# Kernel tuning notes

Measured on AMD Instinct MI355X. Metric: run time of the kernel, lower is better.

The kernel has to match this reference:

```python
import jax, jax.numpy as jnp
import numpy as np

EMBED_DIM = 1024
NUM_HEADS = 16
D_K = EMBED_DIM // NUM_HEADS


def setup_inputs() -> dict:
    key = jax.random.key(0)
    ks = jax.random.split(key, 5)
    x = jax.random.normal(ks[0], (2, 2048, EMBED_DIM), dtype=jnp.float32)
    # kaiming_normal on 2D params: std = sqrt(2/fan_in) with fan_in = in_features
    w_qkv = jax.random.normal(ks[1], (3 * EMBED_DIM, EMBED_DIM), dtype=jnp.float32) * np.sqrt(2.0 / EMBED_DIM)
    b_qkv = jnp.zeros((3 * EMBED_DIM,), dtype=jnp.float32)
    w_o = jax.random.normal(ks[2], (EMBED_DIM, EMBED_DIM), dtype=jnp.float32) * np.sqrt(2.0 / EMBED_DIM)
    b_o = jnp.zeros((EMBED_DIM,), dtype=jnp.float32)
    return {"x": x, "w_qkv": w_qkv, "b_qkv": b_qkv, "w_o": w_o, "b_o": b_o}


def reference(x, w_qkv, b_qkv, w_o, b_o):
    B, N, C = x.shape
    qkv = x @ w_qkv.T + b_qkv  # [B,N,3C]
    q, k, v = jnp.split(qkv, 3, axis=-1)
    # [B,H,N,d_k]
    q = q.reshape(B, N, NUM_HEADS, D_K).transpose(0, 2, 1, 3)
    k = k.reshape(B, N, NUM_HEADS, D_K).transpose(0, 2, 1, 3)
    v = v.reshape(B, N, NUM_HEADS, D_K).transpose(0, 2, 1, 3)
    # NOTE: original forward scales by 1/sqrt(embed_dim), not 1/sqrt(d_k)
    scores = jnp.einsum('bhqd,bhkd->bhqk', q, k) / np.sqrt(C).astype(np.float32)
    causal = jnp.tril(jnp.ones((N, N), dtype=bool))
    scores = jnp.where(causal, scores, -jnp.inf)
    attn = jax.nn.softmax(scores, axis=-1)
    out = jnp.einsum('bhqk,bhkd->bhqd', attn, v)  # [B,H,N,d_k]
    out = out.transpose(0, 2, 1, 3).reshape(B, N, C)
    return out @ w_o.T + b_o
```

## Files before the change

kernel.cpp:

```cpp
#include <hip/hip_runtime.h>
#include <hip/hip_bf16.h>
#include <math.h>

typedef __bf16 bf16_t;
typedef __bf16 bf16x8 __attribute__((ext_vector_type(8)));
typedef __bf16 bf16x4 __attribute__((ext_vector_type(4)));
typedef __bf16 bf16x2 __attribute__((ext_vector_type(2)));
typedef float f32x4 __attribute__((ext_vector_type(4)));
typedef unsigned u32x4 __attribute__((ext_vector_type(4)));

#define SCALE_L2E 0.045084234f
#define ROUND_B 0.0028169f

#define MFMA16(a, b, c) __builtin_amdgcn_mfma_f32_16x16x32_bf16(a, b, c, 0, 0, 0)

__device__ __forceinline__ unsigned pack2(float a, float b) {
  return __builtin_amdgcn_perm(__builtin_bit_cast(unsigned, b),
                               __builtin_bit_cast(unsigned, a), 0x07060302u);
}

__global__ void convert3_f32_bf16(const float* __restrict__ a, int na,
                                  const float* __restrict__ b, int nb,
                                  const float* __restrict__ c, int nc,
                                  bf16_t* __restrict__ oa, bf16_t* __restrict__ ob,
                                  bf16_t* __restrict__ oc) {
  int i = (blockIdx.x * blockDim.x + threadIdx.x) * 8;
  const float* src;
  bf16_t* dst;
  int off;
  if (i < na) { src = a; dst = oa; off = i; }
  else if (i < na + nb) { src = b; dst = ob; off = i - na; }
  else if (i < na + nb + nc) { src = c; dst = oc; off = i - na - nb; }
  else return;
  float4 u = *(const float4*)&src[off];
  float4 v = *(const float4*)&src[off + 4];
  bf16x8 w = {(bf16_t)u.x, (bf16_t)u.y, (bf16_t)u.z, (bf16_t)u.w,
              (bf16_t)v.x, (bf16_t)v.y, (bf16_t)v.z, (bf16_t)v.w};
  *(bf16x8*)&dst[off] = w;
}

#define GLOBAL_AS __attribute__((address_space(1)))
#define LDS_AS __attribute__((address_space(3)))
__device__ __forceinline__ void g2l16(const void* g, void* l) {
  __builtin_amdgcn_global_load_lds((const GLOBAL_AS void*)g, (LDS_AS void*)l,
                                   16, 0, 0);
}

template <typename TC, int BN>
__launch_bounds__(256)
__global__ void gemm_bt_bias(const bf16_t* __restrict__ A,
                             const bf16_t* __restrict__ B,
                             const float* __restrict__ bias,
                             TC* __restrict__ C,
                             int M, int N, int K) {
  constexpr int NT = BN / 32;
  __shared__ bf16_t As[128 * 32];
  __shared__ bf16_t Bs[BN * 32];

  const int t = threadIdx.x;
  const int wave = t >> 6, lane = t & 63, quad = lane >> 4, ln = lane & 15;
  const int wm = (wave >> 1) * 64, wn = (wave & 1) * (BN / 2);
  const int m0 = blockIdx.y * 128, n0 = blockIdx.x * BN;

  const int srow = lane >> 2;
  const int schunk = ((lane & 3) ^ ((lane >> 3) & 3)) * 8;
  const bf16_t* gA0 = &A[(size_t)(m0 + wave * 32 + srow) * K + schunk];
  const bf16_t* gA1 = gA0 + (size_t)16 * K;
  bf16_t* lA0 = &As[(wave * 32) * 32];
  bf16_t* lA1 = &As[(wave * 32 + 16) * 32];
  const bf16_t* gB0 = &B[(size_t)(n0 + (BN == 128 ? wave * 32 : wave * 16) + srow) * K + schunk];
  const bf16_t* gB1 = gB0 + (size_t)16 * K;
  bf16_t* lB0 = &Bs[((BN == 128 ? wave * 32 : wave * 16)) * 32];
  bf16_t* lB1 = &Bs[(wave * 32 + 16) * 32];

  const int cslot = (quad ^ ((ln >> 1) & 3)) * 8;

  f32x4 acc[4][NT];
  for (int i = 0; i < 4; i++)
    for (int j = 0; j < NT; j++) acc[i][j] = (f32x4){0.f, 0.f, 0.f, 0.f};

  for (int k0 = 0; k0 < K; k0 += 32) {
    __syncthreads();
    g2l16(gA0 + k0, lA0);
    g2l16(gA1 + k0, lA1);
    g2l16(gB0 + k0, lB0);
    if (BN == 128) g2l16(gB1 + k0, lB1);
    __syncthreads();

    bf16x8 af[4], bfr[NT];
    for (int mt = 0; mt < 4; mt++)
      af[mt] = *(const bf16x8*)&As[(wm + mt * 16 + ln) * 32 + cslot];
    for (int nt = 0; nt < NT; nt++)
      bfr[nt] = *(const bf16x8*)&Bs[(wn + nt * 16 + ln) * 32 + cslot];
    for (int mt = 0; mt < 4; mt++)
      for (int nt = 0; nt < NT; nt++)
        acc[mt][nt] = MFMA16(af[mt], bfr[nt], acc[mt][nt]);
  }

  for (int nt = 0; nt < NT; nt++) {
    int col = n0 + wn + nt * 16 + ln;
    float bv = bias[col];
    for (int mt = 0; mt < 4; mt++) {
      int row = m0 + wm + mt * 16 + quad * 4;
      for (int r = 0; r < 4; r++)
        C[(size_t)(row + r) * N + col] = (TC)(acc[mt][nt][r] + bv);
    }
  }
}

__launch_bounds__(256, 2)
__global__ void gemm128db(const bf16_t* __restrict__ A,
                          const bf16_t* __restrict__ B,
                          const float* __restrict__ bias,
                          bf16_t* __restrict__ C,
                          int M, int N, int K) {
  __shared__ __align__(16) bf16_t Ab[2][128 * 64];
  __shared__ __align__(16) bf16_t Bb[2][128 * 64];

  const int tid = threadIdx.x;
  const int wave = tid >> 6, lane = tid & 63, quad = lane >> 4, ln = lane & 15;
  const int wm = wave >> 1, wn = wave & 1;
  const int m0 = blockIdx.y * 128, n0 = blockIdx.x * 128;
  const int nt = K >> 6;

  const int rowoff = wave * 8 + (lane >> 3);
  const int c8 = ((lane & 7) ^ (lane >> 3)) * 8;
  const int w8row = wave * 8;
  const bf16_t* Arow0 = A + (size_t)(m0 + rowoff) * K + c8;
  const bf16_t* Brow0 = B + (size_t)(n0 + rowoff) * K + c8;

  auto stA = [&](int tl) {
    const bf16_t* g = Arow0 + (size_t)tl * 64;
    bf16_t* l = &Ab[tl & 1][w8row * 64];
#pragma unroll
    for (int rr = 0; rr < 128; rr += 32)
      g2l16(g + (size_t)rr * K, l + rr * 64);
  };
  auto stB = [&](int tl) {
    const bf16_t* g = Brow0 + (size_t)tl * 64;
    bf16_t* l = &Bb[tl & 1][w8row * 64];
#pragma unroll
    for (int rr = 0; rr < 128; rr += 32)
      g2l16(g + (size_t)rr * K, l + rr * 64);
  };

  const int cswl = (quad ^ (ln & 7)) * 8;
  const int aBase = (wm * 64 + ln) * 64;
  const int bBase = (wn * 64 + ln) * 64;

  f32x4 acc[4][4];
#pragma unroll
  for (int i = 0; i < 4; i++)
#pragma unroll
    for (int j = 0; j < 4; j++) acc[i][j] = (f32x4){0.f, 0.f, 0.f, 0.f};

  bf16x8 af[4][2], bfr[4][2];

  auto ldA = [&](int buf) {
#pragma unroll
    for (int mf = 0; mf < 4; ++mf)
#pragma unroll
      for (int sk = 0; sk < 2; ++sk)
        af[mf][sk] = *(const bf16x8*)&Ab[buf][aBase + mf * 1024 +
                                             (cswl ^ (sk << 5))];
  };
  auto ldB = [&](int buf) {
#pragma unroll
    for (int nf = 0; nf < 4; ++nf)
#pragma unroll
      for (int sk = 0; sk < 2; ++sk)
        bfr[nf][sk] = *(const bf16x8*)&Bb[buf][bBase + nf * 1024 +
                                               (cswl ^ (sk << 5))];
  };
  auto mm = [&]() {
#pragma unroll
    for (int mf = 0; mf < 4; ++mf)
#pragma unroll
      for (int nf = 0; nf < 4; ++nf) {
        f32x4 c = acc[mf][nf];
        c = MFMA16(af[mf][0], bfr[nf][0], c);
        c = MFMA16(af[mf][1], bfr[nf][1], c);
        acc[mf][nf] = c;
      }
  };

  stA(0); stB(0);
  __syncthreads();

  for (int tl = 0; tl < nt; ++tl) {
    const int buf = tl & 1;
    if (tl + 1 < nt) { stA(tl + 1); stB(tl + 1); }
    ldA(buf);
    ldB(buf);
    mm();
    __syncthreads();
  }

#pragma unroll
  for (int nf = 0; nf < 4; ++nf) {
    const int col = n0 + wn * 64 + nf * 16 + ln;
    const float bv = bias[col];
#pragma unroll
    for (int mf = 0; mf < 4; ++mf) {
      const int row = m0 + wm * 64 + mf * 16 + quad * 4;
#pragma unroll
      for (int r = 0; r < 4; ++r)
        C[(size_t)(row + r) * N + col] = (bf16_t)(acc[mf][nf][r] + bv);
    }
  }
}

__launch_bounds__(256, 2)
__global__ void attn_kernel(const bf16_t* __restrict__ qkv,
                            bf16_t* __restrict__ out) {
  constexpr int KP = 72, VP = 72;
  constexpr int BUF = 64 * KP;
  __shared__ __align__(16) bf16_t KsB[2 * BUF];
  __shared__ __align__(16) bf16_t VtB[2 * BUF];

  const int t = threadIdx.x;
  const int wave = t >> 6, lane = t & 63, quad = lane >> 4, ln = lane & 15;
  const int p = blockIdx.x >> 5;
  const int bh = blockIdx.x & 31;
  const int b = bh >> 4, h = bh & 15;
  const int qA = p * 64, qB = (31 - p) * 64;
  const int ntiles = 32 - p;
  const size_t rs = 3072;
  const size_t base = (size_t)b * 2048 * rs;

  const size_t qoffA = base + (size_t)(qA + wave * 16 + ln) * rs + h * 64;
  const size_t qoffB = base + (size_t)(qB + wave * 16 + ln) * rs + h * 64;
  bf16x8 qfA0 = *(const bf16x8*)&qkv[qoffA + quad * 8];
  bf16x8 qfA1 = *(const bf16x8*)&qkv[qoffA + 32 + quad * 8];
  bf16x8 qfB0 = *(const bf16x8*)&qkv[qoffB + quad * 8];
  bf16x8 qfB1 = *(const bf16x8*)&qkv[qoffB + 32 + quad * 8];

  f32x4 oA[4], oB[4];
  f32x4 lAv = (f32x4){0.f, 0.f, 0.f, 0.f};
  f32x4 lBv = (f32x4){0.f, 0.f, 0.f, 0.f};
  for (int ct = 0; ct < 4; ct++) {
    oA[ct] = (f32x4){0.f, 0.f, 0.f, 0.f};
    oB[ct] = (f32x4){0.f, 0.f, 0.f, 0.f};
  }

  const int r0 = t >> 3, c0 = (t & 7) * 8;
  const int ksA = r0 * KP + (((t & 7) + wave) & 7) * 8;
  const int ksB2 = (r0 + 32) * KP + (((t & 7) + wave + 4) & 7) * 8;
  const int vkoff = ((((r0 >> 2) + (t & 7)) & 7)) * 8 + 2 * (r0 & 3);

  const bf16_t* kpa = &qkv[base + 1024 + h * 64 + (size_t)r0 * rs + c0];
  const bf16_t* kpb = kpa + (size_t)32 * rs;
  const bf16_t* vpa = &qkv[base + 2048 + h * 64 + (size_t)(2 * r0) * rs + c0];
  const bf16_t* vpb = vpa + rs;
  const size_t tstep = (size_t)64 * rs;

  bf16x8 ka = *(const bf16x8*)kpa; kpa += tstep;
  bf16x8 kb = *(const bf16x8*)kpb; kpb += tstep;
  bf16x8 va2 = *(const bf16x8*)vpa; vpa += tstep;
  bf16x8 vb2 = *(const bf16x8*)vpb; vpb += tstep;

  const int qgA = qA + wave * 16 + ln;
  const int qgB = qB + wave * 16 + ln;

  auto stage_to = [&](int buf) {
    bf16_t* KsW = &KsB[buf * BUF];
    bf16_t* VtW = &VtB[buf * BUF];
    *(bf16x8*)&KsW[ksA] = ka;
    *(bf16x8*)&KsW[ksB2] = kb;
#pragma unroll
    for (int j = 0; j < 8; j++) {
      bf16x2 w2 = {va2[j], vb2[j]};
      *(bf16x2*)&VtW[(c0 + j) * VP + vkoff] = w2;
    }
  };
  auto prefetch = [&]() {
    ka = *(const bf16x8*)kpa; kpa += tstep;
    kb = *(const bf16x8*)kpb; kpb += tstep;
    va2 = *(const bf16x8*)vpa; vpa += tstep;
    vb2 = *(const bf16x8*)vpb; vpb += tstep;
  };
  auto load_kfs = [&](const bf16_t* Ks, bf16x8* kf0s, bf16x8* kf1s) {
#pragma unroll
    for (int st = 0; st < 4; st++) {
      const int krow = st * 16 + ln;
      const int rot = 2 * st + (ln >> 3);
      kf0s[st] = *(const bf16x8*)&Ks[krow * KP + ((quad + rot) & 7) * 8];
      kf1s[st] = *(const bf16x8*)&Ks[krow * KP + ((quad + 4 + rot) & 7) * 8];
    }
  };
  auto qk_block = [&](const bf16x8* kf0s, const bf16x8* kf1s, bf16x8 q0,
                      bf16x8 q1, f32x4& lxv, bf16x8* Bp, bool masked,
                      int kbase, int qg) {
#pragma unroll
    for (int pr = 0; pr < 2; pr++) {
      u32x4 u;
#pragma unroll
      for (int sh = 0; sh < 2; sh++) {
        const int st = pr * 2 + sh;
        f32x4 s = (f32x4){0.f, 0.f, 0.f, 0.f};
        __builtin_amdgcn_s_setprio(1);
        s = MFMA16(kf0s[st], q0, s);
        s = MFMA16(kf1s[st], q1, s);
        __builtin_amdgcn_s_setprio(0);
        const int k0g = kbase + st * 16 + quad * 4;
        float pv[4];
#pragma unroll
        for (int r = 0; r < 4; r++) {
          float e = __builtin_amdgcn_exp2f(fmaf(s[r], SCALE_L2E, ROUND_B));
          if (masked && (k0g + r > qg)) e = 0.f;
          lxv[r] += e;
          pv[r] = e;
        }
        u[sh * 2] = pack2(pv[0], pv[1]);
        u[sh * 2 + 1] = pack2(pv[2], pv[3]);
      }
      Bp[pr] = __builtin_bit_cast(bf16x8, u);
    }
  };
  auto load_vfs = [&](const bf16_t* Vt, bf16x8* A8s) {
#pragma unroll
    for (int pr = 0; pr < 2; pr++) {
#pragma unroll
      for (int ct = 0; ct < 4; ct++) {
        const int dd = ct * 16 + ln;
        const int bc = (quad >> 1) + 2 * ct + (ln >> 3);
        const int cA = (4 * pr + bc) & 7;
        const int cB = (4 * pr + 2 + bc) & 7;
        bf16x4 v0 = *(const bf16x4*)&Vt[dd * VP + cA * 8 + (quad & 1) * 4];
        bf16x4 v1 = *(const bf16x4*)&Vt[dd * VP + cB * 8 + (quad & 1) * 4];
        A8s[pr * 4 + ct] = __builtin_shufflevector(v0, v1, 0, 1, 2, 3, 4, 5, 6, 7);
      }
    }
  };

  auto body = [&](int kt, bool hasA, bool maskA, bool maskB) {
    if (kt + 1 < ntiles) {
      stage_to((kt + 1) & 1);
      if (kt + 2 < ntiles) prefetch();
    }
    const bf16_t* Ks = &KsB[(kt & 1) * BUF];
    const bf16_t* Vt = &VtB[(kt & 1) * BUF];
    bf16x8 kf0s[4], kf1s[4];
    load_kfs(Ks, kf0s, kf1s);
    bf16x8 BpA[2], BpB[2];
    if (hasA) qk_block(kf0s, kf1s, qfA0, qfA1, lAv, BpA, maskA, kt * 64, qgA);
    qk_block(kf0s, kf1s, qfB0, qfB1, lBv, BpB, maskB, kt * 64, qgB);
    bf16x8 A8s[8];
    load_vfs(Vt, A8s);
    __builtin_amdgcn_s_setprio(1);
#pragma unroll
    for (int pr = 0; pr < 2; pr++) {
#pragma unroll
      for (int ct = 0; ct < 4; ct++) {
        if (hasA) oA[ct] = MFMA16(A8s[pr * 4 + ct], BpA[pr], oA[ct]);
        oB[ct] = MFMA16(A8s[pr * 4 + ct], BpB[pr], oB[ct]);
      }
    }
    __builtin_amdgcn_s_setprio(0);
    if (kt + 1 < ntiles) __syncthreads();
  };

  stage_to(0);
  if (ntiles > 1) prefetch();
  __syncthreads();

  for (int kt = 0; kt < p; kt++) body(kt, true, false, false);
  body(p, true, true, false);
  for (int kt = p + 1; kt < 31 - p; kt++) body(kt, false, false, false);
  body(31 - p, false, false, true);

  float lAx = (lAv[0] + lAv[1]) + (lAv[2] + lAv[3]);
  float lBx = (lBv[0] + lBv[1]) + (lBv[2] + lBv[3]);
  lAx += __shfl_xor(lAx, 16);
  lAx += __shfl_xor(lAx, 32);
  lBx += __shfl_xor(lBx, 16);
  lBx += __shfl_xor(lBx, 32);
  const float invA = __builtin_amdgcn_rcpf(lAx);
  const float invB = __builtin_amdgcn_rcpf(lBx);
  const int ocol = h * 64 + quad * 4;
#pragma unroll
  for (int ct = 0; ct < 4; ct++) {
    bf16x4 wa, wb;
#pragma unroll
    for (int r = 0; r < 4; r++) {
      wa[r] = (bf16_t)(oA[ct][r] * invA);
      wb[r] = (bf16_t)(oB[ct][r] * invB);
    }
    *(bf16x4*)&out[(size_t)(b * 2048 + qgA) * 1024 + ocol + ct * 16] = wa;
    *(bf16x4*)&out[(size_t)(b * 2048 + qgB) * 1024 + ocol + ct * 16] = wb;
  }
}

extern "C" void kernel_launch(void* const* d_in, const int* in_sizes, int n_in,
                              void* d_out, int out_size, void* d_ws, size_t ws_size,
                              hipStream_t stream) {
  const float* x     = (const float*)d_in[0];
  const float* w_qkv = (const float*)d_in[1];
  const float* b_qkv = (const float*)d_in[2];
  const float* w_o   = (const float*)d_in[3];
  const float* b_o   = (const float*)d_in[4];
  float* out = (float*)d_out;

  bf16_t* qkv   = (bf16_t*)d_ws;
  bf16_t* xbf   = qkv + (size_t)4096 * 3072;
  bf16_t* wqkvb = xbf + (size_t)4096 * 1024;
  bf16_t* wob   = wqkvb + (size_t)3072 * 1024;
  bf16_t* attn  = xbf;

  const int na = 4096 * 1024, nb = 3072 * 1024, nc = 1024 * 1024;
  convert3_f32_bf16<<<dim3((na + nb + nc) / (256 * 8)), 256, 0, stream>>>(
      x, na, w_qkv, nb, w_o, nc, xbf, wqkvb, wob);

  gemm128db<<<dim3(3072 / 128, 4096 / 128), 256, 0, stream>>>(
      xbf, wqkvb, b_qkv, qkv, 4096, 3072, 1024);
  attn_kernel<<<dim3(512), 256, 0, stream>>>(qkv, attn);
  gemm_bt_bias<float, 64><<<dim3(1024 / 64, 4096 / 128), 256, 0, stream>>>(
      attn, wob, b_o, out, 4096, 1024, 1024);
}
```

Before: 177.7 us.

## Split each attention key tile across two wave groups with LDS reduction

The attention block grows from 256 to 512 threads, and each half of the waves handles half of every 64-key tile. In the global-to-LDS staging, one half loads K and the other loads V. Each half now computes half the QK and PV MFMAs per tile, holding fewer K/V fragments per wave. The halves' partial outputs and row sums are combined through LDS at the end. The goal is more waves per CU to hide latency and shorter per-wave dependency chains, at the cost of an extra barrier, an LDS reduction, and a tighter register budget under the new launch bounds.

```diff
diff --git a/kernel.cpp b/kernel.cpp
--- a/kernel.cpp
+++ b/kernel.cpp
@@ -210,7 +210,7 @@
   }
 }
 
-__launch_bounds__(256, 2)
+__launch_bounds__(512, 4)
 __global__ void attn_kernel(const bf16_t* __restrict__ qkv,
                             bf16_t* __restrict__ out) {
   constexpr int KP = 72, VP = 72;
@@ -220,6 +220,8 @@
 
   const int t = threadIdx.x;
   const int wave = t >> 6, lane = t & 63, quad = lane >> 4, ln = lane & 15;
+  const int qw = wave & 3;
+  const int kh = wave >> 2;
   const int p = blockIdx.x >> 5;
   const int bh = blockIdx.x & 31;
   const int b = bh >> 4, h = bh & 15;
@@ -228,8 +230,8 @@
   const size_t rs = 3072;
   const size_t base = (size_t)b * 2048 * rs;
 
-  const size_t qoffA = base + (size_t)(qA + wave * 16 + ln) * rs + h * 64;
-  const size_t qoffB = base + (size_t)(qB + wave * 16 + ln) * rs + h * 64;
+  const size_t qoffA = base + (size_t)(qA + qw * 16 + ln) * rs + h * 64;
+  const size_t qoffB = base + (size_t)(qB + qw * 16 + ln) * rs + h * 64;
   bf16x8 qfA0 = *(const bf16x8*)&qkv[qoffA + quad * 8];
   bf16x8 qfA1 = *(const bf16x8*)&qkv[qoffA + 32 + quad * 8];
   bf16x8 qfB0 = *(const bf16x8*)&qkv[qoffB + quad * 8];
@@ -243,93 +245,93 @@
     oB[ct] = (f32x4){0.f, 0.f, 0.f, 0.f};
   }
 
-  const int r0 = t >> 3, c0 = (t & 7) * 8;
-  const int ksA = r0 * KP + (((t & 7) + wave) & 7) * 8;
-  const int ksB2 = (r0 + 32) * KP + (((t & 7) + wave + 4) & 7) * 8;
-  const int vkoff = ((((r0 >> 2) + (t & 7)) & 7)) * 8 + 2 * (r0 & 3);
-
-  const bf16_t* kpa = &qkv[base + 1024 + h * 64 + (size_t)r0 * rs + c0];
-  const bf16_t* kpb = kpa + (size_t)32 * rs;
-  const bf16_t* vpa = &qkv[base + 2048 + h * 64 + (size_t)(2 * r0) * rs + c0];
-  const bf16_t* vpb = vpa + rs;
+  const int t256 = t & 255;
+  const int r0 = t256 >> 3, c0 = (t256 & 7) * 8;
+  const int wav4 = t256 >> 6;
+  const int ksA = r0 * KP + (((t256 & 7) + wav4) & 7) * 8;
+  const int ksB2 = (r0 + 32) * KP + (((t256 & 7) + wav4 + 4) & 7) * 8;
+  const int vkoff = ((((r0 >> 2) + (t256 & 7)) & 7)) * 8 + 2 * (r0 & 3);
+
+  const bf16_t* gp0;
+  const bf16_t* gp1;
+  if (kh) {
+    gp0 = &qkv[base + 1024 + h * 64 + (size_t)r0 * rs + c0];
+    gp1 = gp0 + (size_t)32 * rs;
+  } else {
+    gp0 = &qkv[base + 2048 + h * 64 + (size_t)(2 * r0) * rs + c0];
+    gp1 = gp0 + rs;
+  }
   const size_t tstep = (size_t)64 * rs;
 
-  bf16x8 ka = *(const bf16x8*)kpa; kpa += tstep;
-  bf16x8 kb = *(const bf16x8*)kpb; kpb += tstep;
-  bf16x8 va2 = *(const bf16x8*)vpa; vpa += tstep;
-  bf16x8 vb2 = *(const bf16x8*)vpb; vpb += tstep;
-
-  const int qgA = qA + wave * 16 + ln;
-  const int qgB = qB + wave * 16 + ln;
+  bf16x8 s0 = *(const bf16x8*)gp0; gp0 += tstep;
+  bf16x8 s1 = *(const bf16x8*)gp1; gp1 += tstep;
+
+  const int qgA = qA + qw * 16 + ln;
+  const int qgB = qB + qw * 16 + ln;
 
   auto stage_to = [&](int buf) {
-    bf16_t* KsW = &KsB[buf * BUF];
-    bf16_t* VtW = &VtB[buf * BUF];
-    *(bf16x8*)&KsW[ksA] = ka;
-    *(bf16x8*)&KsW[ksB2] = kb;
-#pragma unroll
-    for (int j = 0; j < 8; j++) {
-      bf16x2 w2 = {va2[j], vb2[j]};
-      *(bf16x2*)&VtW[(c0 + j) * VP + vkoff] = w2;
+    if (kh) {
+      bf16_t* KsW = &KsB[buf * BUF];
+      *(bf16x8*)&KsW[ksA] = s0;
+      *(bf16x8*)&KsW[ksB2] = s1;
+    } else {
+      bf16_t* VtW = &VtB[buf * BUF];
+#pragma unroll
+      for (int j = 0; j < 8; j++) {
+        bf16x2 w2 = {s0[j], s1[j]};
+        *(bf16x2*)&VtW[(c0 + j) * VP + vkoff] = w2;
+      }
     }
   };
   auto prefetch = [&]() {
-    ka = *(const bf16x8*)kpa; kpa += tstep;
-    kb = *(const bf16x8*)kpb; kpb += tstep;
-    va2 = *(const bf16x8*)vpa; vpa += tstep;
-    vb2 = *(const bf16x8*)vpb; vpb += tstep;
+    s0 = *(const bf16x8*)gp0; gp0 += tstep;
+    s1 = *(const bf16x8*)gp1; gp1 += tstep;
   };
   auto load_kfs = [&](const bf16_t* Ks, bf16x8* kf0s, bf16x8* kf1s) {
 #pragma unroll
-    for (int st = 0; st < 4; st++) {
+    for (int sh = 0; sh < 2; sh++) {
+      const int st = kh * 2 + sh;
       const int krow = st * 16 + ln;
       const int rot = 2 * st + (ln >> 3);
-      kf0s[st] = *(const bf16x8*)&Ks[krow * KP + ((quad + rot) & 7) * 8];
-      kf1s[st] = *(const bf16x8*)&Ks[krow * KP + ((quad + 4 + rot) & 7) * 8];
+      kf0s[sh] = *(const bf16x8*)&Ks[krow * KP + ((quad + rot) & 7) * 8];
+      kf1s[sh] = *(const bf16x8*)&Ks[krow * KP + ((quad + 4 + rot) & 7) * 8];
     }
   };
   auto qk_block = [&](const bf16x8* kf0s, const bf16x8* kf1s, bf16x8 q0,
-                      bf16x8 q1, f32x4& lxv, bf16x8* Bp, bool masked,
+                      bf16x8 q1, f32x4& lxv, bf16x8& Bp, bool masked,
                       int kbase, int qg) {
-#pragma unroll
-    for (int pr = 0; pr < 2; pr++) {
-      u32x4 u;
-#pragma unroll
-      for (int sh = 0; sh < 2; sh++) {
-        const int st = pr * 2 + sh;
-        f32x4 s = (f32x4){0.f, 0.f, 0.f, 0.f};
-        __builtin_amdgcn_s_setprio(1);
-        s = MFMA16(kf0s[st], q0, s);
-        s = MFMA16(kf1s[st], q1, s);
-        __builtin_amdgcn_s_setprio(0);
-        const int k0g = kbase + st * 16 + quad * 4;
-        float pv[4];
-#pragma unroll
-        for (int r = 0; r < 4; r++) {
-          float e = __builtin_amdgcn_exp2f(fmaf(s[r], SCALE_L2E, ROUND_B));
-          if (masked && (k0g + r > qg)) e = 0.f;
-          lxv[r] += e;
-          pv[r] = e;
-        }
-        u[sh * 2] = pack2(pv[0], pv[1]);
-        u[sh * 2 + 1] = pack2(pv[2], pv[3]);
+    u32x4 u;
+#pragma unroll
+    for (int sh = 0; sh < 2; sh++) {
+      f32x4 s = (f32x4){0.f, 0.f, 0.f, 0.f};
+      __builtin_amdgcn_s_setprio(1);
+      s = MFMA16(kf0s[sh], q0, s);
+      s = MFMA16(kf1s[sh], q1, s);
+      __builtin_amdgcn_s_setprio(0);
+      const int k0g = kbase + (kh * 2 + sh) * 16 + quad * 4;
+      float pv[4];
+#pragma unroll
+      for (int r = 0; r < 4; r++) {
+        float e = __builtin_amdgcn_exp2f(fmaf(s[r], SCALE_L2E, ROUND_B));
+        if (masked && (k0g + r > qg)) e = 0.f;
+        lxv[r] += e;
+        pv[r] = e;
       }
-      Bp[pr] = __builtin_bit_cast(bf16x8, u);
-    }
+      u[sh * 2] = pack2(pv[0], pv[1]);
+      u[sh * 2 + 1] = pack2(pv[2], pv[3]);
+    }
+    Bp = __builtin_bit_cast(bf16x8, u);
   };
   auto load_vfs = [&](const bf16_t* Vt, bf16x8* A8s) {
 #pragma unroll
-    for (int pr = 0; pr < 2; pr++) {
-#pragma unroll
-      for (int ct = 0; ct < 4; ct++) {
-        const int dd = ct * 16 + ln;
-        const int bc = (quad >> 1) + 2 * ct + (ln >> 3);
-        const int cA = (4 * pr + bc) & 7;
-        const int cB = (4 * pr + 2 + bc) & 7;
-        bf16x4 v0 = *(const bf16x4*)&Vt[dd * VP + cA * 8 + (quad & 1) * 4];
-        bf16x4 v1 = *(const bf16x4*)&Vt[dd * VP + cB * 8 + (quad & 1) * 4];
-        A8s[pr * 4 + ct] = __builtin_shufflevector(v0, v1, 0, 1, 2, 3, 4, 5, 6, 7);
-      }
+    for (int ct = 0; ct < 4; ct++) {
+      const int dd = ct * 16 + ln;
+      const int bc = (quad >> 1) + 2 * ct + (ln >> 3);
+      const int cA = (4 * kh + bc) & 7;
+      const int cB = (4 * kh + 2 + bc) & 7;
+      bf16x4 v0 = *(const bf16x4*)&Vt[dd * VP + cA * 8 + (quad & 1) * 4];
+      bf16x4 v1 = *(const bf16x4*)&Vt[dd * VP + cB * 8 + (quad & 1) * 4];
+      A8s[ct] = __builtin_shufflevector(v0, v1, 0, 1, 2, 3, 4, 5, 6, 7);
     }
   };
 
@@ -340,21 +342,18 @@
     }
     const bf16_t* Ks = &KsB[(kt & 1) * BUF];
     const bf16_t* Vt = &VtB[(kt & 1) * BUF];
-    bf16x8 kf0s[4], kf1s[4];
+    bf16x8 kf0s[2], kf1s[2];
     load_kfs(Ks, kf0s, kf1s);
-    bf16x8 BpA[2], BpB[2];
+    bf16x8 BpA, BpB;
     if (hasA) qk_block(kf0s, kf1s, qfA0, qfA1, lAv, BpA, maskA, kt * 64, qgA);
     qk_block(kf0s, kf1s, qfB0, qfB1, lBv, BpB, maskB, kt * 64, qgB);
-    bf16x8 A8s[8];
+    bf16x8 A8s[4];
     load_vfs(Vt, A8s);
     __builtin_amdgcn_s_setprio(1);
 #pragma unroll
-    for (int pr = 0; pr < 2; pr++) {
-#pragma unroll
-      for (int ct = 0; ct < 4; ct++) {
-        if (hasA) oA[ct] = MFMA16(A8s[pr * 4 + ct], BpA[pr], oA[ct]);
-        oB[ct] = MFMA16(A8s[pr * 4 + ct], BpB[pr], oB[ct]);
-      }
+    for (int ct = 0; ct < 4; ct++) {
+      if (hasA) oA[ct] = MFMA16(A8s[ct], BpA, oA[ct]);
+      oB[ct] = MFMA16(A8s[ct], BpB, oB[ct]);
     }
     __builtin_amdgcn_s_setprio(0);
     if (kt + 1 < ntiles) __syncthreads();
@@ -375,19 +374,43 @@
   lAx += __shfl_xor(lAx, 32);
   lBx += __shfl_xor(lBx, 16);
   lBx += __shfl_xor(lBx, 32);
-  const float invA = __builtin_amdgcn_rcpf(lAx);
-  const float invB = __builtin_amdgcn_rcpf(lBx);
-  const int ocol = h * 64 + quad * 4;
-#pragma unroll
-  for (int ct = 0; ct < 4; ct++) {
-    bf16x4 wa, wb;
-#pragma unroll
-    for (int r = 0; r < 4; r++) {
-      wa[r] = (bf16_t)(oA[ct][r] * invA);
-      wb[r] = (bf16_t)(oB[ct][r] * invB);
-    }
-    *(bf16x4*)&out[(size_t)(b * 2048 + qgA) * 1024 + ocol + ct * 16] = wa;
-    *(bf16x4*)&out[(size_t)(b * 2048 + qgB) * 1024 + ocol + ct * 16] = wb;
+
+  __syncthreads();
+  float* redA = (float*)KsB;
+  float* redB = (float*)VtB;
+  const int idx = qw * 64 + lane;
+  if (kh) {
+#pragma unroll
+    for (int ct = 0; ct < 4; ct++) {
+      *(f32x4*)&redA[(ct * 256 + idx) * 4] = oA[ct];
+      *(f32x4*)&redB[(ct * 256 + idx) * 4] = oB[ct];
+    }
+    redA[4096 + idx] = lAx;
+    redB[4096 + idx] = lBx;
+  }
+  __syncthreads();
+  if (!kh) {
+#pragma unroll
+    for (int ct = 0; ct < 4; ct++) {
+      oA[ct] += *(const f32x4*)&redA[(ct * 256 + idx) * 4];
+      oB[ct] += *(const f32x4*)&redB[(ct * 256 + idx) * 4];
+    }
+    lAx += redA[4096 + idx];
+    lBx += redB[4096 + idx];
+    const float invA = __builtin_amdgcn_rcpf(lAx);
+    const float invB = __builtin_amdgcn_rcpf(lBx);
+    const int ocol = h * 64 + quad * 4;
+#pragma unroll
+    for (int ct = 0; ct < 4; ct++) {
+      bf16x4 wa, wb;
+#pragma unroll
+      for (int r = 0; r < 4; r++) {
+        wa[r] = (bf16_t)(oA[ct][r] * invA);
+        wb[r] = (bf16_t)(oB[ct][r] * invB);
+      }
+      *(bf16x4*)&out[(size_t)(b * 2048 + qgA) * 1024 + ocol + ct * 16] = wa;
+      *(bf16x4*)&out[(size_t)(b * 2048 + qgB) * 1024 + ocol + ct * 16] = wb;
+    }
   }
 }
 
@@ -413,7 +436,7 @@
 
   gemm128db<<<dim3(3072 / 128, 4096 / 128), 256, 0, stream>>>(
       xbf, wqkvb, b_qkv, qkv, 4096, 3072, 1024);
-  attn_kernel<<<dim3(512), 256, 0, stream>>>(qkv, attn);
+  attn_kernel<<<dim3(512), 512, 0, stream>>>(qkv, attn);
   gemm_bt_bias<float, 64><<<dim3(1024 / 64, 4096 / 128), 256, 0, stream>>>(
       attn, wob, b_o, out, 4096, 1024, 1024);
 }
```

After: 177.4 us. No clear change (-0.2%).
